# Kernel tuning notes

Hardware: AMD Instinct MI355X
Metric: run time of the kernel (lower is better)

Reference implementation:

```python
import jax, jax.numpy as jnp
import numpy as np

B, N, M, K, S, P, H, W = 8, 32, 32, 3, 1, 1, 192, 192
NH = (H + 2 * P - K) // S + 1
NW = (W + 2 * P - K) // S + 1


def setup_inputs() -> dict:
    key = jax.random.key(0)
    ks = jax.random.split(key, 8)
    f = lambda k, sh, sc: jax.random.normal(k, sh, jnp.float32) * sc
    return {
        "x": f(ks[0], (B, N, H, W), 1.0),
        "a1_w": f(ks[1], (K * K, N, K, K), 0.05),  # attention1 conv k x k
        "a1_b": jnp.zeros((K * K,), jnp.float32),
        "a2_w": f(ks[2], (K * K, K * K), 0.1),      # attention1 1x1 conv
        "a2_b": jnp.zeros((K * K,), jnp.float32),
        "a3_w": f(ks[3], (K * K, K * K), 0.1),      # attention1 1x1 conv
        "a3_b": jnp.zeros((K * K,), jnp.float32),
        "b1_w": f(ks[4], (M, N), 0.05),             # attention3 1x1 conv
        "b1_b": jnp.zeros((M,), jnp.float32),
        "b2_w": f(ks[5], (M, M), 0.05),             # attention3 1x1 conv
        "b2_b": jnp.zeros((M,), jnp.float32),
        "weight": f(ks[6], (M, N, K, K), 0.05),     # main conv weight
    }


def _attention1(x, a1_w, a1_b, a2_w, a2_b, a3_w, a3_b):
    # Conv(k) -> ReLU -> Conv1x1 -> ReLU -> Conv1x1 -> Sigmoid; out [B, K*K, NH, NW]
    a = jax.lax.conv_general_dilated(
        x, a1_w, (S, S), [(P, P), (P, P)],
        dimension_numbers=("NCHW", "OIHW", "NCHW"))
    a = jax.nn.relu(a + a1_b[None, :, None, None])
    a = jax.nn.relu(jnp.einsum("oi,bihw->bohw", a2_w, a) + a2_b[None, :, None, None])
    a = jnp.einsum("oi,bihw->bohw", a3_w, a) + a3_b[None, :, None, None]
    return jax.nn.sigmoid(a)


def _unfold(x):
    # torch F.unfold ordering: channel-major, kernel positions inner.
    # returns [B, N, K*K, NH, NW]
    xp = jnp.pad(x, ((0, 0), (0, 0), (P, P), (P, P)))
    cols = [xp[:, :, i:i + (NH - 1) * S + 1:S, j:j + (NW - 1) * S + 1:S]
            for i in range(K) for j in range(K)]
    return jnp.stack(cols, axis=2)


def reference(x, a1_w, a1_b, a2_w, a2_b, a3_w, a3_b, b1_w, b1_b, b2_w, b2_b, weight):
    att = _attention1(x, a1_w, a1_b, a2_w, a2_b, a3_w, a3_b)  # [B, K*K, NH, NW]
    pat = _unfold(x)                                          # [B, N, K*K, NH, NW]
    w = weight.reshape(M, N, K * K)
    # attention-weighted unfold + matmul + fold, fused as one einsum
    y = jnp.einsum("bnphw,bphw,mnp->bmhw", pat, att, w)       # [B, M, NH, NW]
    # attention3 bias: global avg pool -> 1x1 -> ReLU -> 1x1
    pooled = x.mean(axis=(2, 3))                              # [B, N]
    h = jax.nn.relu(pooled @ b1_w.T + b1_b)
    bias = h @ b2_w.T + b2_b                                  # [B, M]
    return y + bias[:, :, None, None]
```

## Files before the change

### kernel.cpp

```cpp
#include <hip/hip_runtime.h>
#include <math.h>

#define B_ 8
#define N_ 32
#define M_ 32
#define HW 192

typedef __attribute__((ext_vector_type(8))) short short8;
typedef __attribute__((ext_vector_type(4))) float float4_;

__device__ inline unsigned short f2bf(float f) {
    unsigned int b = __float_as_uint(f);
    b += 0x7FFF + ((b >> 16) & 1);
    return (unsigned short)(b >> 16);
}
__device__ inline float bf2f(unsigned short u) {
    return __uint_as_float((unsigned int)u << 16);
}

union U8 { short8 s; unsigned int u[4]; };

__global__ __launch_bounds__(192) void transpose_pool_kernel(
    const float* __restrict__ x, const float* __restrict__ a1w,
    const float* __restrict__ weight, float* __restrict__ partial,
    unsigned short* __restrict__ a1A, unsigned short* __restrict__ wA,
    unsigned short* __restrict__ xt) {
    const int id = blockIdx.x;
    const int tid = threadIdx.x;
    if (id == 1536) {
        for (int idx = tid; idx < 9 * 512; idx += 192) {
            int j = idx & 7, l = (idx >> 3) & 63, c = idx >> 9;
            int o = l & 15, n = (l >> 4) * 8 + j;
            float v = (o < 9) ? a1w[(o * N_ + n) * 9 + c] : 0.f;
            a1A[idx] = f2bf(v);
        }
        for (int idx = tid; idx < 9 * 1024; idx += 192) {
            int j = idx & 7, l = (idx >> 3) & 63, mt = (idx >> 9) & 1, c = idx >> 10;
            int m = mt * 16 + (l & 15), n = (l >> 4) * 8 + j;
            wA[idx] = f2bf(weight[(m * N_ + n) * 9 + c]);
        }
        return;
    }
    const int b = id & 7, h = id >> 3;
    const float* xb = x + (size_t)b * N_ * (HW * HW) + h * HW + tid;
    float v[32];
#pragma unroll
    for (int n = 0; n < 32; ++n) v[n] = xb[n * (HW * HW)];
    U8 tq[4];
#pragma unroll
    for (int q = 0; q < 4; ++q)
#pragma unroll
        for (int i = 0; i < 4; ++i)
            tq[q].u[i] = (unsigned)f2bf(v[q * 8 + 2 * i]) |
                         ((unsigned)f2bf(v[q * 8 + 2 * i + 1]) << 16);
    short8* dst = (short8*)&xt[(((size_t)b * HW + h) * HW + tid) * 32];
    dst[0] = tq[0].s; dst[1] = tq[1].s; dst[2] = tq[2].s; dst[3] = tq[3].s;

    __shared__ float red[3][32];
    const int wv = tid >> 6, lane = tid & 63;
#pragma unroll
    for (int n = 0; n < 32; ++n) {
        float s = v[n];
#pragma unroll
        for (int off = 32; off > 0; off >>= 1) s += __shfl_down(s, off, 64);
        if (lane == 0) red[wv][n] = s;
    }
    __syncthreads();
    if (tid < 32)
        partial[((size_t)b * HW + h) * 32 + tid] =
            red[0][tid] + red[1][tid] + red[2][tid];
}

__global__ __launch_bounds__(256, 6) void laconv_kernel(
    const unsigned short* __restrict__ xt, const float* __restrict__ a1b,
    const float* __restrict__ a2w, const float* __restrict__ a2b,
    const float* __restrict__ a3w, const float* __restrict__ a3b,
    const unsigned short* __restrict__ a1A, const unsigned short* __restrict__ wA,
    const float* __restrict__ partial, const float* __restrict__ b1w,
    const float* __restrict__ b1b, const float* __restrict__ b2w,
    const float* __restrict__ b2b, float* __restrict__ out) {
    __shared__ __align__(16) unsigned short xs[4 * 324 * 8];
    __shared__ unsigned short att_s[9 * 264];
    __shared__ float pooled_s[N_], hsh[M_];
    __shared__ __align__(16) float bias_lds[M_];

    const int id = blockIdx.x;
    const int b = id & 7;
    const int t = id >> 3;
    const int bx = t % 12, by = t / 12;
    const int th0 = by * 16, tw0 = bx * 16;
    const int tid = threadIdx.x;
    const int wv = tid >> 6, lane = tid & 63;
    const int tx = lane & 15, ks = lane >> 4;

    const unsigned short* xtb = xt + (size_t)b * (HW * HW) * 32;
    short8 ra[4], rb[4];
    {
        int pos = tid, r = pos / 18, cc = pos - r * 18;
        int h = th0 + r - 1, w = tw0 + cc - 1;
        if (((unsigned)h < HW) && ((unsigned)w < HW)) {
            const short8* src = (const short8*)&xtb[(size_t)(h * HW + w) * 32];
            ra[0] = src[0]; ra[1] = src[1]; ra[2] = src[2]; ra[3] = src[3];
        } else {
#pragma unroll
            for (int g = 0; g < 4; ++g) ra[g] = (short8)(short)0;
        }
    }
    const bool hasB = tid < 324 - 256;
    if (hasB) {
        int pos = 256 + tid, r = pos / 18, cc = pos - r * 18;
        int h = th0 + r - 1, w = tw0 + cc - 1;
        if (((unsigned)h < HW) && ((unsigned)w < HW)) {
            const short8* src = (const short8*)&xtb[(size_t)(h * HW + w) * 32];
            rb[0] = src[0]; rb[1] = src[1]; rb[2] = src[2]; rb[3] = src[3];
        } else {
#pragma unroll
            for (int g = 0; g < 4; ++g) rb[g] = (short8)(short)0;
        }
    }
    float ps = 0.f;
    if (tid < N_) {
        for (int c = 0; c < HW; ++c) ps += partial[((size_t)b * HW + c) * 32 + tid];
    }
#pragma unroll
    for (int g = 0; g < 4; ++g) *(short8*)&xs[g * 2592 + tid * 8] = ra[g];
    if (hasB) {
#pragma unroll
        for (int g = 0; g < 4; ++g) *(short8*)&xs[g * 2592 + (256 + tid) * 8] = rb[g];
    }
    if (tid < N_) pooled_s[tid] = ps * (1.f / (HW * HW));
    __syncthreads();

    if (tid < M_) {
        float s = b1b[tid];
#pragma unroll
        for (int n = 0; n < N_; n++) s += pooled_s[n] * b1w[tid * N_ + n];
        hsh[tid] = fmaxf(s, 0.f);
    }

    const int pb = ks * 2592 + wv * 576 + tx * 8;
    const float4_ zero4 = {0.f, 0.f, 0.f, 0.f};

    float4_ aacc[4];
#pragma unroll
    for (int g = 0; g < 4; ++g) aacc[g] = zero4;
#pragma unroll
    for (int c = 0; c < 9; ++c) {
        short8 aA = ((const short8*)a1A)[c * 64 + lane];
        const int coff = (c / 3) * 144 + (c % 3) * 8;
#pragma unroll
        for (int g = 0; g < 4; ++g) {
            short8 bP = *(const short8*)&xs[pb + g * 144 + coff];
            aacc[g] = __builtin_amdgcn_mfma_f32_16x16x32_bf16(aA, bP, aacc[g], 0, 0, 0);
        }
    }
#pragma unroll
    for (int g = 0; g < 4; ++g) {
#pragma unroll
        for (int reg = 0; reg < 4; ++reg) {
            int o = ks * 4 + reg;
            if (o < 9) att_s[o * 264 + (wv * 4 + g) * 16 + tx] = f2bf(aacc[g][reg]);
        }
    }
    __syncthreads();

    if (tid < M_) {
        float s2 = b2b[tid];
#pragma unroll
        for (int q = 0; q < M_; q++) s2 += hsh[q] * b2w[tid * M_ + q];
        bias_lds[tid] = s2;
    }

    float t1[9], t2[9], attv[9];
#pragma unroll
    for (int o = 0; o < 9; ++o)
        t1[o] = fmaxf(bf2f(att_s[o * 264 + tid]) + a1b[o], 0.f);
#pragma unroll
    for (int o2 = 0; o2 < 9; ++o2) {
        float s = a2b[o2];
#pragma unroll
        for (int o = 0; o < 9; ++o) s += a2w[o2 * 9 + o] * t1[o];
        t2[o2] = fmaxf(s, 0.f);
    }
#pragma unroll
    for (int o3 = 0; o3 < 9; ++o3) {
        float s = a3b[o3];
#pragma unroll
        for (int o2 = 0; o2 < 9; ++o2) s += a3w[o3 * 9 + o2] * t2[o2];
        attv[o3] = 1.f / (1.f + __expf(-s));
    }
#pragma unroll
    for (int p = 0; p < 9; ++p) att_s[p * 264 + tid] = f2bf(attv[p]);
    __syncthreads();

    float4_ acc0[4], acc1[4];
#pragma unroll
    for (int g = 0; g < 4; ++g) { acc0[g] = zero4; acc1[g] = zero4; }
#pragma unroll
    for (int c = 0; c < 9; ++c) {
        short8 w0 = ((const short8*)wA)[c * 128 + lane];
        short8 w1 = ((const short8*)wA)[c * 128 + 64 + lane];
        const int coff = (c / 3) * 144 + (c % 3) * 8;
#pragma unroll
        for (int g = 0; g < 4; ++g) {
            short8 bP = *(const short8*)&xs[pb + g * 144 + coff];
            float av = bf2f(att_s[c * 264 + (wv * 4 + g) * 16 + tx]);
            float4_ av4 = {av, av, av, av};
            float4_ z0 = __builtin_amdgcn_mfma_f32_16x16x32_bf16(w0, bP, zero4, 0, 0, 0);
            float4_ z1 = __builtin_amdgcn_mfma_f32_16x16x32_bf16(w1, bP, zero4, 0, 0, 0);
            acc0[g] = acc0[g] + av4 * z0;
            acc1[g] = acc1[g] + av4 * z1;
        }
    }

    const int wc = tw0 + tx;
    float4_ bv0 = *(const float4_*)&bias_lds[ks * 4];
    float4_ bv1 = *(const float4_*)&bias_lds[16 + ks * 4];
#pragma unroll
    for (int g = 0; g < 4; ++g) {
        int h = th0 + wv * 4 + g;
#pragma unroll
        for (int reg = 0; reg < 4; ++reg) {
            int m0 = ks * 4 + reg;
            out[((b * M_ + m0) * HW + h) * HW + wc] = acc0[g][reg] + bv0[reg];
            out[((b * M_ + m0 + 16) * HW + h) * HW + wc] = acc1[g][reg] + bv1[reg];
        }
    }
}

extern "C" void kernel_launch(void* const* d_in, const int* in_sizes, int n_in,
                              void* d_out, int out_size, void* d_ws,
                              size_t ws_size, hipStream_t stream) {
    const float* x   = (const float*)d_in[0];
    const float* a1w = (const float*)d_in[1];
    const float* a1b = (const float*)d_in[2];
    const float* a2w = (const float*)d_in[3];
    const float* a2b = (const float*)d_in[4];
    const float* a3w = (const float*)d_in[5];
    const float* a3b = (const float*)d_in[6];
    const float* b1w = (const float*)d_in[7];
    const float* b1b = (const float*)d_in[8];
    const float* b2w = (const float*)d_in[9];
    const float* b2b = (const float*)d_in[10];
    const float* wgt = (const float*)d_in[11];
    float* out = (float*)d_out;

    char* ws = (char*)d_ws;
    float* partial       = (float*)(ws);
    unsigned short* a1A  = (unsigned short*)(ws + 196608);
    unsigned short* wAf  = (unsigned short*)(ws + 205824);
    unsigned short* xt   = (unsigned short*)(ws + 262144);

    transpose_pool_kernel<<<dim3(B_ * HW + 1), dim3(192), 0, stream>>>(
        x, a1w, wgt, partial, a1A, wAf, xt);
    laconv_kernel<<<dim3(12 * 12 * B_), dim3(256), 0, stream>>>(
        xt, a1b, a2w, a2b, a3w, a3b, a1A, wAf, partial, b1w, b1b, b2w, b2b, out);
    (void)in_sizes; (void)n_in; (void)out_size; (void)ws_size;
}
```

Before: 152.1 us.

## Hoist pooled bias MLP into separate kernel and reshape tiles to 8x32

Moves the global-pool reduction and the two small bias MLP layers out of every laconv block into a single one-block bias_kernel, so each tile no longer redundantly sums 192 partial rows and runs two 32x32 matvecs. The spatial tile changes from 16x16 to 8 rows by 32 columns. Each wave's MFMA groups now cover half-rows, and the LDS halo layout grows from 18x18 to 10x34. Wider tiles give longer contiguous output stores per row, at the cost of a larger halo ratio and an extra kernel launch. The launch_bounds occupancy hint is also dropped.

```diff
diff --git a/kernel.cpp b/kernel.cpp
--- a/kernel.cpp
+++ b/kernel.cpp
@@ -71,32 +71,54 @@
             red[0][tid] + red[1][tid] + red[2][tid];
 }
 
-__global__ __launch_bounds__(256, 6) void laconv_kernel(
+__global__ __launch_bounds__(256) void bias_kernel(
+    const float* __restrict__ partial, const float* __restrict__ b1w,
+    const float* __restrict__ b1b, const float* __restrict__ b2w,
+    const float* __restrict__ b2b, float* __restrict__ bias) {
+    const int tid = threadIdx.x;
+    const int b = tid >> 5, j = tid & 31;
+    float ps = 0.f;
+#pragma unroll 8
+    for (int h = 0; h < HW; ++h) ps += partial[((size_t)b * HW + h) * 32 + j];
+    __shared__ float pooled_s[B_][32], hsh[B_][32];
+    pooled_s[b][j] = ps * (1.f / (HW * HW));
+    __syncthreads();
+    float s = b1b[j];
+#pragma unroll
+    for (int n = 0; n < N_; ++n) s += pooled_s[b][n] * b1w[j * N_ + n];
+    hsh[b][j] = fmaxf(s, 0.f);
+    __syncthreads();
+    float s2 = b2b[j];
+#pragma unroll
+    for (int q = 0; q < M_; ++q) s2 += hsh[b][q] * b2w[j * M_ + q];
+    bias[b * M_ + j] = s2;
+}
+
+__global__ __launch_bounds__(256) void laconv_kernel(
     const unsigned short* __restrict__ xt, const float* __restrict__ a1b,
     const float* __restrict__ a2w, const float* __restrict__ a2b,
     const float* __restrict__ a3w, const float* __restrict__ a3b,
     const unsigned short* __restrict__ a1A, const unsigned short* __restrict__ wA,
-    const float* __restrict__ partial, const float* __restrict__ b1w,
-    const float* __restrict__ b1b, const float* __restrict__ b2w,
-    const float* __restrict__ b2b, float* __restrict__ out) {
-    __shared__ __align__(16) unsigned short xs[4 * 324 * 8];
+    const float* __restrict__ bias, float* __restrict__ out) {
+    __shared__ __align__(16) unsigned short xs[4 * 2728];
     __shared__ unsigned short att_s[9 * 264];
-    __shared__ float pooled_s[N_], hsh[M_];
-    __shared__ __align__(16) float bias_lds[M_];
 
     const int id = blockIdx.x;
     const int b = id & 7;
     const int t = id >> 3;
-    const int bx = t % 12, by = t / 12;
-    const int th0 = by * 16, tw0 = bx * 16;
+    const int bx = t % 6, by = t / 6;
+    const int th0 = by * 8, tw0 = bx * 32;
     const int tid = threadIdx.x;
     const int wv = tid >> 6, lane = tid & 63;
     const int tx = lane & 15, ks = lane >> 4;
 
+    float4_ bv0 = *(const float4_*)&bias[b * M_ + ks * 4];
+    float4_ bv1 = *(const float4_*)&bias[b * M_ + 16 + ks * 4];
+
     const unsigned short* xtb = xt + (size_t)b * (HW * HW) * 32;
     short8 ra[4], rb[4];
     {
-        int pos = tid, r = pos / 18, cc = pos - r * 18;
+        int pos = tid, r = pos / 34, cc = pos - r * 34;
         int h = th0 + r - 1, w = tw0 + cc - 1;
         if (((unsigned)h < HW) && ((unsigned)w < HW)) {
             const short8* src = (const short8*)&xtb[(size_t)(h * HW + w) * 32];
@@ -106,9 +128,9 @@
             for (int g = 0; g < 4; ++g) ra[g] = (short8)(short)0;
         }
     }
-    const bool hasB = tid < 324 - 256;
+    const bool hasB = tid < 340 - 256;
     if (hasB) {
-        int pos = 256 + tid, r = pos / 18, cc = pos - r * 18;
+        int pos = 256 + tid, r = pos / 34, cc = pos - r * 34;
         int h = th0 + r - 1, w = tw0 + cc - 1;
         if (((unsigned)h < HW) && ((unsigned)w < HW)) {
             const short8* src = (const short8*)&xtb[(size_t)(h * HW + w) * 32];
@@ -118,27 +140,20 @@
             for (int g = 0; g < 4; ++g) rb[g] = (short8)(short)0;
         }
     }
-    float ps = 0.f;
-    if (tid < N_) {
-        for (int c = 0; c < HW; ++c) ps += partial[((size_t)b * HW + c) * 32 + tid];
-    }
-#pragma unroll
-    for (int g = 0; g < 4; ++g) *(short8*)&xs[g * 2592 + tid * 8] = ra[g];
+#pragma unroll
+    for (int g = 0; g < 4; ++g) *(short8*)&xs[g * 2728 + tid * 8] = ra[g];
     if (hasB) {
 #pragma unroll
-        for (int g = 0; g < 4; ++g) *(short8*)&xs[g * 2592 + (256 + tid) * 8] = rb[g];
-    }
-    if (tid < N_) pooled_s[tid] = ps * (1.f / (HW * HW));
-    __syncthreads();
-
-    if (tid < M_) {
-        float s = b1b[tid];
-#pragma unroll
-        for (int n = 0; n < N_; n++) s += pooled_s[n] * b1w[tid * N_ + n];
-        hsh[tid] = fmaxf(s, 0.f);
-    }
-
-    const int pb = ks * 2592 + wv * 576 + tx * 8;
+        for (int g = 0; g < 4; ++g) *(short8*)&xs[g * 2728 + (256 + tid) * 8] = rb[g];
+    }
+    __syncthreads();
+
+    int pbg[4];
+#pragma unroll
+    for (int g = 0; g < 4; ++g) {
+        int gi = wv * 4 + g;
+        pbg[g] = ks * 2728 + (((gi >> 1)) * 34 + ((gi & 1) << 4) + tx) * 8;
+    }
     const float4_ zero4 = {0.f, 0.f, 0.f, 0.f};
 
     float4_ aacc[4];
@@ -147,10 +162,10 @@
 #pragma unroll
     for (int c = 0; c < 9; ++c) {
         short8 aA = ((const short8*)a1A)[c * 64 + lane];
-        const int coff = (c / 3) * 144 + (c % 3) * 8;
+        const int coff = (c / 3) * 272 + (c % 3) * 8;
 #pragma unroll
         for (int g = 0; g < 4; ++g) {
-            short8 bP = *(const short8*)&xs[pb + g * 144 + coff];
+            short8 bP = *(const short8*)&xs[pbg[g] + coff];
             aacc[g] = __builtin_amdgcn_mfma_f32_16x16x32_bf16(aA, bP, aacc[g], 0, 0, 0);
         }
     }
@@ -164,13 +179,6 @@
     }
     __syncthreads();
 
-    if (tid < M_) {
-        float s2 = b2b[tid];
-#pragma unroll
-        for (int q = 0; q < M_; q++) s2 += hsh[q] * b2w[tid * M_ + q];
-        bias_lds[tid] = s2;
-    }
-
     float t1[9], t2[9], attv[9];
 #pragma unroll
     for (int o = 0; o < 9; ++o)
@@ -200,10 +208,10 @@
     for (int c = 0; c < 9; ++c) {
         short8 w0 = ((const short8*)wA)[c * 128 + lane];
         short8 w1 = ((const short8*)wA)[c * 128 + 64 + lane];
-        const int coff = (c / 3) * 144 + (c % 3) * 8;
+        const int coff = (c / 3) * 272 + (c % 3) * 8;
 #pragma unroll
         for (int g = 0; g < 4; ++g) {
-            short8 bP = *(const short8*)&xs[pb + g * 144 + coff];
+            short8 bP = *(const short8*)&xs[pbg[g] + coff];
             float av = bf2f(att_s[c * 264 + (wv * 4 + g) * 16 + tx]);
             float4_ av4 = {av, av, av, av};
             float4_ z0 = __builtin_amdgcn_mfma_f32_16x16x32_bf16(w0, bP, zero4, 0, 0, 0);
@@ -213,12 +221,11 @@
         }
     }
 
-    const int wc = tw0 + tx;
-    float4_ bv0 = *(const float4_*)&bias_lds[ks * 4];
-    float4_ bv1 = *(const float4_*)&bias_lds[16 + ks * 4];
 #pragma unroll
     for (int g = 0; g < 4; ++g) {
-        int h = th0 + wv * 4 + g;
+        int gi = wv * 4 + g;
+        int h = th0 + (gi >> 1);
+        int wc = tw0 + ((gi & 1) << 4) + tx;
 #pragma unroll
         for (int reg = 0; reg < 4; ++reg) {
             int m0 = ks * 4 + reg;
@@ -249,11 +256,14 @@
     float* partial       = (float*)(ws);
     unsigned short* a1A  = (unsigned short*)(ws + 196608);
     unsigned short* wAf  = (unsigned short*)(ws + 205824);
+    float* biasv         = (float*)(ws + 224256);
     unsigned short* xt   = (unsigned short*)(ws + 262144);
 
     transpose_pool_kernel<<<dim3(B_ * HW + 1), dim3(192), 0, stream>>>(
         x, a1w, wgt, partial, a1A, wAf, xt);
+    bias_kernel<<<dim3(1), dim3(256), 0, stream>>>(partial, b1w, b1b, b2w, b2b,
+                                                   biasv);
     laconv_kernel<<<dim3(12 * 12 * B_), dim3(256), 0, stream>>>(
-        xt, a1b, a2w, a2b, a3w, a3b, a1A, wAf, partial, b1w, b1b, b2w, b2b, out);
+        xt, a1b, a2w, a2b, a3w, a3b, a1A, wAf, biasv, out);
     (void)in_sizes; (void)n_in; (void)out_size; (void)ws_size;
 }
```

Result: no change. 150.8 us (-0.8%).
